# Performance work log

Measured on AMD Instinct MI355X. Metric: run time of the kernel, lower is better.

## Reference

```python
import jax, jax.numpy as jnp
import numpy as np

NDIM, NINEQ, NEQ = 1024, 512, 256
EPS = 1e-4       # Q regularization (module's eps)
N_ITERS = 25     # fixed primal-dual interior-point iterations
SIGMA = 0.1      # centering parameter


def setup_inputs() -> dict:
    key = jax.random.key(0)
    ks = jax.random.split(key, 5)
    L = jnp.tril(jax.random.uniform(ks[0], (NDIM, NDIM)))                      # tril(rand) as in torch init
    q = jax.random.uniform(ks[1], (NDIM,), minval=-1.0, maxval=1.0)
    G = jax.random.uniform(ks[2], (NINEQ, NDIM), minval=-1.0, maxval=1.0)
    A = jax.random.uniform(ks[3], (NEQ, NDIM), minval=-1.0, maxval=1.0)
    b = jax.random.uniform(ks[4], (NEQ,), minval=-1.0, maxval=1.0)
    x0 = jnp.zeros((NDIM,), jnp.float32)   # nn.Parameter(torch.zeros(ndim))
    s0 = jnp.ones((NINEQ,), jnp.float32)   # nn.Parameter(torch.ones(nineq))
    return {"L": L, "q": q, "G": G, "A": A, "b": b, "x0": x0, "s0": s0}


def _frac_to_boundary(v, dv):
    # max step alpha in (0,1] keeping v + alpha*dv > 0, with 0.99 backoff
    safe_dv = jnp.where(dv < 0, dv, -1.0)
    ratio = jnp.where(dv < 0, -v / safe_dv, 1.0)
    return jnp.min(ratio)


def _solve_qp(Q, q, G, h, A, b):
    n, m, p = q.shape[0], h.shape[0], b.shape[0]

    def step(state, _):
        x, s, z, y = state
        r_x = Q @ x + q + G.T @ z + A.T @ y          # dual residual
        r_p = G @ x + s - h                           # primal ineq residual
        r_y = A @ x - b                               # primal eq residual
        mu = jnp.dot(s, z) / m
        r_c = s * z - SIGMA * mu                      # centered complementarity
        D = z / s                                     # diag scaling
        H = Q + G.T @ (D[:, None] * G)                # reduced Hessian [n,n]
        KKT = jnp.block([[H, A.T], [A, jnp.zeros((p, p), Q.dtype)]])
        rhs = jnp.concatenate([-(r_x + G.T @ ((-r_c + z * r_p) / s)), -r_y])
        sol = jnp.linalg.solve(KKT, rhs)
        dx, dy = sol[:n], sol[n:]
        ds = -r_p - G @ dx
        dz = (-r_c - z * ds) / s
        alpha = 0.99 * jnp.minimum(1.0, jnp.minimum(_frac_to_boundary(s, ds), _frac_to_boundary(z, dz)))
        return (x + alpha * dx, s + alpha * ds, z + alpha * dz, y + alpha * dy), None

    init = (jnp.zeros((n,), Q.dtype), jnp.ones((m,), Q.dtype), jnp.ones((m,), Q.dtype), jnp.zeros((p,), Q.dtype))
    (x, s, z, y), _ = jax.lax.scan(step, init, None, length=N_ITERS)
    return x


def reference(L, q, G, A, b, x0, s0):
    Lt = jnp.tril(L)  # M * L with M = tril(ones)
    Q = Lt @ Lt.T + EPS * jnp.eye(L.shape[0], dtype=L.dtype)
    h = G @ x0 + s0   # learn_h branch (source's self.z0 is self.x0)
    return _solve_qp(Q, q, G, h, A, b)
```

## Files before the change

### kernel.cpp

```cpp
#include <hip/hip_runtime.h>
#include <hip/hip_bf16.h>


constexpr int ND = 1024;
constexpr int MI = 512;
constexpr int PE = 256;
constexpr int NM = 512;
constexpr int LDM = 520;
constexpr double EPSQ = 1e-4;
constexpr double SIG = 0.1;
constexpr int NITER = 25;

__device__ __forceinline__ double wred(double v) {
#pragma unroll
  for (int off = 32; off; off >>= 1) v += __shfl_down(v, off, 64);
  return v;
}

__global__ void k_prep(const float* __restrict__ Gf, const float* __restrict__ Af,
                       const float* __restrict__ qf, const float* __restrict__ bf,
                       float* __restrict__ GTf, float* __restrict__ ATf,
                       double* __restrict__ qd, double* __restrict__ bd,
                       double* __restrict__ xv, double* __restrict__ sv,
                       double* __restrict__ zv, double* __restrict__ yv,
// ... 18 lines not shown
  if (wid >= MI) return;
  double acc = 0;
  for (int c = lane; c < ND; c += 64) acc += (double)Gf[(size_t)wid * ND + c] * (double)x0f[c];
  acc = wred(acc);
  if (lane == 0) hd[wid] = acc + (double)s0f[wid];
}

__global__ __launch_bounds__(256) void k_qbuild(const float* __restrict__ Lf,
                                                double* __restrict__ Qd, double* __restrict__ LQ) {
  __shared__ double As[32][33], Bs[32][33];
  int i0 = blockIdx.y * 32, j0 = blockIdx.x * 32;
  int tx = threadIdx.x & 15, ty = threadIdx.x >> 4;
  double acc[2][2] = {};
  int kmax = (i0 < j0 ? i0 : j0) + 32;
  for (int k0 = 0; k0 < kmax; k0 += 32) {
    for (int l = threadIdx.x; l < 1024; l += 256) {
      int r = l >> 5, c = l & 31;
      As[r][c] = (k0 + c <= i0 + r) ? (double)Lf[(size_t)(i0 + r) * ND + k0 + c] : 0.0;
      Bs[r][c] = (k0 + c <= j0 + r) ? (double)Lf[(size_t)(j0 + r) * ND + k0 + c] : 0.0;
    }
    __syncthreads();
#pragma unroll
    for (int k = 0; k < 32; k++) {
      double a0 = As[2 * ty][k], a1 = As[2 * ty + 1][k];
      double b0 = Bs[2 * tx][k], b1 = Bs[2 * tx + 1][k];
      acc[0][0] += a0 * b0; acc[0][1] += a0 * b1;
      acc[1][0] += a1 * b0; acc[1][1] += a1 * b1;
    }
    __syncthreads();
  }
  for (int da = 0; da < 2; da++)
    for (int db = 0; db < 2; db++) {
      int i = i0 + 2 * ty + da, j = j0 + 2 * tx + db;
      double v = acc[da][db] + (i == j ? EPSQ : 0.0);
      Qd[(size_t)i * ND + j] = v;
      LQ[(size_t)i * ND + j] = v;
    }
}

__global__ __launch_bounds__(256) void k_chol_diag_inv(double* __restrict__ A, int lda, int kb,
                                                       double* __restrict__ DG) {
  __shared__ double a[64][65];
  __shared__ double invp[2080];
  __shared__ double dfloor;
  int t = threadIdx.x;
  size_t base = (size_t)kb * 64;
  for (int l = t; l < 4096; l += 256) { int r = l >> 6, c = l & 63; a[r][c] = A[(base + r) * lda + base + c]; }
  __syncthreads();
  if (t == 0) {
    double m = 0;
    for (int i = 0; i < 64; i++) m = fmax(m, fabs(a[i][i]));
    dfloor = m * 1e-28 + 1e-280;
  }
  __syncthreads();
  for (int j = 0; j < 64; j++) {
    if (t == 0) a[j][j] = sqrt(fmax(a[j][j], dfloor));
    __syncthreads();
    double piv = a[j][j];
    for (int r = j + 1 + t; r < 64; r += 256) a[r][j] /= piv;
    __syncthreads();
    int w = 63 - j;
    for (int l = t; l < w * w; l += 256) {
      int rr = j + 1 + l / w, cc = j + 1 + l % w;
      if (cc <= rr) a[rr][cc] -= a[rr][j] * a[cc][j];
    }
    __syncthreads();
  }
  for (int l = t; l < 4096; l += 256) { int r = l >> 6, c = l & 63; if (c <= r) A[(base + r) * lda + base + c] = a[r][c]; }
  if (t < 64) {
    int c = t;
    for (int i = c; i < 64; i++) {
      double v = (i == c) ? 1.0 : 0.0;
      for (int k = c; k < i; k++) v -= a[i][k] * invp[k * (k + 1) / 2 + c];
      invp[i * (i + 1) / 2 + c] = v / a[i][i];
    }
  }
  __syncthreads();
  for (int l = t; l < 4096; l += 256) {
    int r = l >> 6, c = l & 63;
    DG[(size_t)kb * 4096 + (size_t)c * 64 + r] = (c <= r) ? invp[r * (r + 1) / 2 + c] : 0.0;
  }
}

__global__ __launch_bounds__(256) void k_fps(double* __restrict__ A, int lda,
                                             double* __restrict__ PL, int ldp,
                                             double* __restrict__ DG, int kb) {
  extern __shared__ double sh[];
  double* DT = sh;
  double* Bs = sh + 4096;
  double* Pi = sh + 8256;
  double* Pj = sh + 12416;
  const int t = threadIdx.x;
  int idx = blockIdx.x;
  int bi = (int)((sqrtf(8.0f * (float)idx + 1.0f) - 1.0f) * 0.5f);
  while ((bi + 1) * (bi + 2) / 2 <= idx) ++bi;
  while (bi * (bi + 1) / 2 > idx) --bi;
  int bj = idx - bi * (bi + 1) / 2;
  const int ib = kb + 1 + bi, jb = kb + 1 + bj;
  const int tx = t & 15, ty = t >> 4;

  for (int l = t; l < 4096; l += 256) DT[l] = DG[(size_t)kb * 4096 + l];
  for (int l = t; l < 4096; l += 256) { int r = l >> 6, c = l & 63; Bs[r * 65 + c] = A[(size_t)(ib * 64 + r) * lda + kb * 64 + c]; }
  __syncthreads();
  {
    double acc[4][4] = {};
    for (int k = 0; k < 64; ++k) {
      double b0 = Bs[ty * 65 + k], b1 = Bs[(ty + 16) * 65 + k];
      double b2 = Bs[(ty + 32) * 65 + k], b3 = Bs[(ty + 48) * 65 + k];
      double d0 = DT[k * 64 + tx], d1 = DT[k * 64 + tx + 16];
      double d2 = DT[k * 64 + tx + 32], d3 = DT[k * 64 + tx + 48];
      acc[0][0] += b0 * d0; acc[0][1] += b0 * d1; acc[0][2] += b0 * d2; acc[0][3] += b0 * d3;
      acc[1][0] += b1 * d0; acc[1][1] += b1 * d1; acc[1][2] += b1 * d2; acc[1][3] += b1 * d3;
      acc[2][0] += b2 * d0; acc[2][1] += b2 * d1; acc[2][2] += b2 * d2; acc[2][3] += b2 * d3;
      acc[3][0] += b3 * d0; acc[3][1] += b3 * d1; acc[3][2] += b3 * d2; acc[3][3] += b3 * d3;
    }
    __syncthreads();
    for (int e = 0; e < 4; ++e)
      for (int f = 0; f < 4; ++f) Pi[(ty + 16 * e) * 65 + tx + 16 * f] = acc[e][f];
  }
  __syncthreads();
  if (ib == jb) {
    for (int l = t; l < 4096; l += 256) {
      int r = l >> 6, c = l & 63;
      PL[(size_t)(ib * 64 + r) * ldp + kb * 64 + c] = Pi[r * 65 + c];
    }
    double* a = Pj;
    {
      double acc[4][4] = {};
      for (int k = 0; k < 64; ++k) {
        double p0 = Pi[ty * 65 + k], p1 = Pi[(ty + 16) * 65 + k];
        double p2 = Pi[(ty + 32) * 65 + k], p3 = Pi[(ty + 48) * 65 + k];
        double q0 = Pi[tx * 65 + k], q1 = Pi[(tx + 16) * 65 + k];
        double q2 = Pi[(tx + 32) * 65 + k], q3 = Pi[(tx + 48) * 65 + k];
        acc[0][0] += p0 * q0; acc[0][1] += p0 * q1; acc[0][2] += p0 * q2; acc[0][3] += p0 * q3;
        acc[1][0] += p1 * q0; acc[1][1] += p1 * q1; acc[1][2] += p1 * q2; acc[1][3] += p1 * q3;
        acc[2][0] += p2 * q0; acc[2][1] += p2 * q1; acc[2][2] += p2 * q2; acc[2][3] += p2 * q3;
        acc[3][0] += p3 * q0; acc[3][1] += p3 * q1; acc[3][2] += p3 * q2; acc[3][3] += p3 * q3;
      }
      for (int e = 0; e < 4; ++e)
        for (int f = 0; f < 4; ++f) {
          int r = ty + 16 * e, c = tx + 16 * f;
          a[r * 65 + c] = A[(size_t)(ib * 64 + r) * lda + jb * 64 + c] - acc[e][f];
        }
    }
    __syncthreads();
    if (ib == kb + 1) {
      if (t == 0) {
        double m = 0;
        for (int i = 0; i < 64; i++) m = fmax(m, fabs(a[i * 65 + i]));
        sh[16576] = m * 1e-28 + 1e-280;
      }
      __syncthreads();
      double dfloor = sh[16576];
      for (int j = 0; j < 64; ++j) {
        if (t == 0) a[j * 65 + j] = sqrt(fmax(a[j * 65 + j], dfloor));
        __syncthreads();
        double piv = a[j * 65 + j];
        for (int r = j + 1 + t; r < 64; r += 256) a[r * 65 + j] /= piv;
        __syncthreads();
        int w = 63 - j;
        for (int l = t; l < w * w; l += 256) {
          int rr = j + 1 + l / w, cc = j + 1 + l % w;
          if (cc <= rr) a[rr * 65 + cc] -= a[rr * 65 + j] * a[cc * 65 + j];
        }
        __syncthreads();
      }
      double* invp = Bs;
      if (t < 64) {
        int c = t;
        for (int i = c; i < 64; ++i) {
          double v = (i == c) ? 1.0 : 0.0;
          for (int k = c; k < i; ++k) v -= a[i * 65 + k] * invp[k * (k + 1) / 2 + c];
          invp[i * (i + 1) / 2 + c] = v / a[i * 65 + i];
        }
      }
      __syncthreads();
      for (int l = t; l < 4096; l += 256) {
        int r = l >> 6, c = l & 63;
        DG[(size_t)(kb + 1) * 4096 + (size_t)c * 64 + r] = (c <= r) ? invp[r * (r + 1) / 2 + c] : 0.0;
      }
    } else {
      for (int l = t; l < 4096; l += 256) {
        int r = l >> 6, c = l & 63;
        A[(size_t)(ib * 64 + r) * lda + jb * 64 + c] = a[r * 65 + c];
      }
    }
  } else {
    for (int l = t; l < 4096; l += 256) { int r = l >> 6, c = l & 63; Bs[r * 65 + c] = A[(size_t)(jb * 64 + r) * lda + kb * 64 + c]; }
    __syncthreads();
    {
      double acc[4][4] = {};
      for (int k = 0; k < 64; ++k) {
        double b0 = Bs[ty * 65 + k], b1 = Bs[(ty + 16) * 65 + k];
        double b2 = Bs[(ty + 32) * 65 + k], b3 = Bs[(ty + 48) * 65 + k];
        double d0 = DT[k * 64 + tx], d1 = DT[k * 64 + tx + 16];
        double d2 = DT[k * 64 + tx + 32], d3 = DT[k * 64 + tx + 48];
        acc[0][0] += b0 * d0; acc[0][1] += b0 * d1; acc[0][2] += b0 * d2; acc[0][3] += b0 * d3;
        acc[1][0] += b1 * d0; acc[1][1] += b1 * d1; acc[1][2] += b1 * d2; acc[1][3] += b1 * d3;
        acc[2][0] += b2 * d0; acc[2][1] += b2 * d1; acc[2][2] += b2 * d2; acc[2][3] += b2 * d3;
        acc[3][0] += b3 * d0; acc[3][1] += b3 * d1; acc[3][2] += b3 * d2; acc[3][3] += b3 * d3;
      }
      __syncthreads();
      for (int e = 0; e < 4; ++e)
        for (int f = 0; f < 4; ++f) Pj[(ty + 16 * e) * 65 + tx + 16 * f] = acc[e][f];
    }
    __syncthreads();
    double acc[4][4] = {};
    for (int k = 0; k < 64; ++k) {
      double p0 = Pi[ty * 65 + k], p1 = Pi[(ty + 16) * 65 + k];
      double p2 = Pi[(ty + 32) * 65 + k], p3 = Pi[(ty + 48) * 65 + k];
      double q0 = Pj[tx * 65 + k], q1 = Pj[(tx + 16) * 65 + k];
      double q2 = Pj[(tx + 32) * 65 + k], q3 = Pj[(tx + 48) * 65 + k];
      acc[0][0] += p0 * q0; acc[0][1] += p0 * q1; acc[0][2] += p0 * q2; acc[0][3] += p0 * q3;
      acc[1][0] += p1 * q0; acc[1][1] += p1 * q1; acc[1][2] += p1 * q2; acc[1][3] += p1 * q3;
      acc[2][0] += p2 * q0; acc[2][1] += p2 * q1; acc[2][2] += p2 * q2; acc[2][3] += p2 * q3;
      acc[3][0] += p3 * q0; acc[3][1] += p3 * q1; acc[3][2] += p3 * q2; acc[3][3] += p3 * q3;
    }
    for (int e = 0; e < 4; ++e)
      for (int f = 0; f < 4; ++f) {
        int r = ty + 16 * e, c = tx + 16 * f;
        size_t off = (size_t)(ib * 64 + r) * lda + jb * 64 + c;
        A[off] -= acc[e][f];
      }
  }
}

__global__ __launch_bounds__(256) void k_trsmf_g(const double* __restrict__ Lm, int lda,
                                                 double* __restrict__ X, int ldx,
                                                 const double* __restrict__ DG, int kb) {
  __shared__ double Lb[64][64];
  __shared__ double Xs[64][33];
  int t = threadIdx.x;
  int c0 = blockIdx.x * 32;
  int lane2 = t & 31, rbase = t >> 5;
  int row0 = kb * 64;
  double acc[8];
#pragma unroll
  for (int e = 0; e < 8; e++) acc[e] = (row0 + rbase + 8 * e == c0 + lane2) ? 1.0 : 0.0;
  for (int jb = 0; jb < kb; jb++) {
    for (int l = t; l < 4096; l += 256) { int r = l >> 6, c = l & 63; Lb[r][c] = Lm[(size_t)(row0 + r) * lda + jb * 64 + c]; }
    for (int l = t; l < 2048; l += 256) { int k = l >> 5, c = l & 31; Xs[k][c] = X[(size_t)(jb * 64 + k) * ldx + c0 + c]; }
    __syncthreads();
#pragma unroll 4
    for (int k = 0; k < 64; k++) {
      double wv = Xs[k][lane2];
#pragma unroll
      for (int e = 0; e < 8; e++) acc[e] -= Lb[rbase + 8 * e][k] * wv;
    }
    __syncthreads();
  }
  __syncthreads();
#pragma unroll
  for (int e = 0; e < 8; e++) Xs[rbase + 8 * e][lane2] = acc[e];
  for (int l = t; l < 4096; l += 256) Lb[l >> 6][l & 63] = DG[(size_t)kb * 4096 + l];
  __syncthreads();
#pragma unroll
  for (int e = 0; e < 8; e++) {
    int i = rbase + 8 * e;
    double s = 0;
#pragma unroll 4
    for (int k = 0; k < 64; k++) s += Lb[k][i] * Xs[k][lane2];
    X[(size_t)(row0 + i) * ldx + c0 + lane2] = s;
  }
}

__global__ __launch_bounds__(256) void k_trsmb_g(const double* __restrict__ Lm, int lda,
                                                 double* __restrict__ X, int ldx,
                                                 const double* __restrict__ DG, int kb, int nkb) {
  __shared__ double Lb[64][64];
  __shared__ double Xs[64][33];
  int t = threadIdx.x;
  int c0 = blockIdx.x * 32;
  int lane2 = t & 31, rbase = t >> 5;
  int row0 = kb * 64;
  double acc[8];
#pragma unroll
  for (int e = 0; e < 8; e++) acc[e] = X[(size_t)(row0 + rbase + 8 * e) * ldx + c0 + lane2];
  for (int jb = kb + 1; jb < nkb; jb++) {
    for (int l = t; l < 4096; l += 256) { int r = l >> 6, c = l & 63; Lb[r][c] = Lm[(size_t)(jb * 64 + r) * lda + kb * 64 + c]; }
    for (int l = t; l < 2048; l += 256) { int k = l >> 5, c = l & 31; Xs[k][c] = X[(size_t)(jb * 64 + k) * ldx + c0 + c]; }
    __syncthreads();
#pragma unroll 4
    for (int k = 0; k < 64; k++) {
      double wv = Xs[k][lane2];
#pragma unroll
      for (int e = 0; e < 8; e++) acc[e] -= Lb[k][rbase + 8 * e] * wv;
    }
    __syncthreads();
  }
  __syncthreads();
#pragma unroll
  for (int e = 0; e < 8; e++) Xs[rbase + 8 * e][lane2] = acc[e];
  for (int l = t; l < 4096; l += 256) Lb[l >> 6][l & 63] = DG[(size_t)kb * 4096 + l];
  __syncthreads();
#pragma unroll
  for (int e = 0; e < 8; e++) {
    int i = rbase + 8 * e;
    double s = 0;
#pragma unroll 4
    for (int k = 0; k < 64; k++) s += Lb[i][k] * Xs[k][lane2];
    X[(size_t)(row0 + i) * ldx + c0 + lane2] = s;
  }
}

__global__ __launch_bounds__(256) void k_aqi(const float* __restrict__ Af, const double* __restrict__ Qi,
                                             double* __restrict__ AQi) {
// ... 127 lines not shown
    }
    __syncthreads();
  }
  for (int da = 0; da < 2; da++)
    for (int db = 0; db < 2; db++)
      FK0x[(size_t)(g0 + 2 * ty + da) * ND + j0 + 2 * tx + db] = acc[da][db];
}

__global__ __launch_bounds__(256) void k_fk0y(const float* __restrict__ Gf, const double* __restrict__ XY,
                                              double* __restrict__ FK0y) {
  __shared__ double As[32][33], Bs[32][33];
  int b0 = blockIdx.x * 32, g0 = blockIdx.y * 32;
  int tx = threadIdx.x & 15, ty = threadIdx.x >> 4;
  double acc[2][2] = {};
  for (int k0 = 0; k0 < ND; k0 += 32) {
    for (int l = threadIdx.x; l < 1024; l += 256) {
      int r = l >> 5, c = l & 31;
      As[r][c] = (double)Gf[(size_t)(g0 + r) * ND + k0 + c];
      Bs[r][c] = XY[(size_t)(k0 + r) * PE + b0 + c];
    }
    __syncthreads();
#pragma unroll
    for (int k = 0; k < 32; k++) {
      double a0v = As[2 * ty][k], a1v = As[2 * ty + 1][k];
      double b0v = Bs[k][2 * tx], b1v = Bs[k][2 * tx + 1];
      acc[0][0] += a0v * b0v; acc[0][1] += a0v * b1v;
      acc[1][0] += a1v * b0v; acc[1][1] += a1v * b1v;
    }
    __syncthreads();
  }
  for (int da = 0; da < 2; da++)
    for (int db = 0; db < 2; db++)
      FK0y[(size_t)(g0 + 2 * ty + da) * PE + b0 + 2 * tx + db] = acc[da][db];
}

__global__ __launch_bounds__(256) void k_smat(const double* __restrict__ FK0x, const float* __restrict__ Gf,
                                              double* __restrict__ S) {
  __shared__ double As[32][33], Bs[32][33];
  int g0 = blockIdx.y * 32, h0 = blockIdx.x * 32;
  int tx = threadIdx.x & 15, ty = threadIdx.x >> 4;
  double acc[2][2] = {};
  for (int k0 = 0; k0 < ND; k0 += 32) {
    for (int l = threadIdx.x; l < 1024; l += 256) {
      int r = l >> 5, c = l & 31;
      As[r][c] = FK0x[(size_t)(g0 + r) * ND + k0 + c];
      Bs[r][c] = (double)Gf[(size_t)(h0 + r) * ND + k0 + c];
    }
    __syncthreads();
#pragma unroll
    for (int k = 0; k < 32; k++) {
      double a0v = As[2 * ty][k], a1v = As[2 * ty + 1][k];
      double b0v = Bs[2 * tx][k], b1v = Bs[2 * tx + 1][k];
      acc[0][0] += a0v * b0v; acc[0][1] += a0v * b1v;
      acc[1][0] += a1v * b0v; acc[1][1] += a1v * b1v;
    }
    __syncthreads();
  }
  for (int da = 0; da < 2; da++)
    for (int db = 0; db < 2; db++)
      S[(size_t)(g0 + 2 * ty + da) * MI + h0 + 2 * tx + db] = acc[da][db];
}

__global__ __launch_bounds__(256) void k_tr(const double* __restrict__ src, double* __restrict__ dst,
                                            int R, int Cc) {
  __shared__ double tile[32][33];
  int r0 = blockIdx.y * 32, c0 = blockIdx.x * 32;
  for (int l = threadIdx.x; l < 1024; l += 256) {
    int r = l >> 5, c = l & 31;
    tile[r][c] = src[(size_t)(r0 + r) * Cc + c0 + c];
  }
  __syncthreads();
  for (int l = threadIdx.x; l < 1024; l += 256) {
    int r = l >> 5, c = l & 31;
    dst[(size_t)(c0 + r) * R + r0 + c] = tile[c][r];
  }
}

__global__ __launch_bounds__(256) void k_A1(const double* __restrict__ Qd, const float* __restrict__ Gf,
                                            const float* __restrict__ Af, const float* __restrict__ GTf,
                                            const float* __restrict__ ATf, const double* __restrict__ qd,
                                            const double* __restrict__ bd, const double* __restrict__ hd,
                                            const double* __restrict__ xv, const double* __restrict__ sv,
                                            const double* __restrict__ zv, const double* __restrict__ yv,
                                            const double* __restrict__ scal,
                                            double* __restrict__ rxv, double* __restrict__ rp,
                                            double* __restrict__ ry, double* __restrict__ uv,
                                            double* __restrict__ dinv) {
  int lane = threadIdx.x & 63;
  if (blockIdx.x < 256) {
    int wid = blockIdx.x * 4 + (int)(threadIdx.x >> 6);
    double acc = 0;
    for (int k = lane; k < ND; k += 64) acc += Qd[(size_t)wid * ND + k] * xv[k];
    for (int k = lane; k < MI; k += 64) acc += (double)GTf[(size_t)wid * MI + k] * zv[k];
    for (int k = lane; k < PE; k += 64) acc += (double)ATf[(size_t)wid * PE + k] * yv[k];
    acc = wred(acc);
    if (lane == 0) rxv[wid] = acc + qd[wid];
  } else {
    int wid = (blockIdx.x - 256) * 4 + (int)(threadIdx.x >> 6);
    if (wid < MI) {
      double acc = 0;
      for (int c = lane; c < ND; c += 64) acc += (double)Gf[(size_t)wid * ND + c] * xv[c];
      acc = wred(acc);
      if (lane == 0) {
        double s0 = sv[wid], z0 = zv[wid];
        double rpv = acc + s0 - hd[wid];
        rp[wid] = rpv;
        double rc0 = s0 * z0 - SIG * scal[0];
        uv[wid] = (-rc0 + z0 * rpv) / s0;
        dinv[wid] = s0 / z0;
      }
    } else {
      int r = wid - MI;
      double acc = 0;
      for (int c = lane; c < ND; c += 64) acc += (double)Af[(size_t)r * ND + c] * xv[c];
      acc = wred(acc);
      if (lane == 0) ry[r] = acc - bd[r];
    }
  }
}

__global__ __launch_bounds__(256) void k_A2(const double* __restrict__ rxv, const float* __restrict__ GTf,
                                            const double* __restrict__ uv, const double* __restrict__ dinv,
                                            const double* __restrict__ ry, const double* __restrict__ S,
                                            const double* __restrict__ FK0x, const double* __restrict__ FK0y,
                                            double* __restrict__ rhs1, double* __restrict__ Mm) {
  int t = threadIdx.x, lane = t & 63;
  if (blockIdx.x < 256) {
    int wid = blockIdx.x * 4 + (t >> 6);
    double acc = 0;
    for (int k = lane; k < MI; k += 64) acc += (double)GTf[(size_t)wid * MI + k] * uv[k];
    acc = wred(acc);
    if (lane == 0) rhs1[wid] = -(rxv[wid] + acc);
  } else if (blockIdx.x < 320) {
    int rbase = (blockIdx.x - 256) * 8;
    for (int rr = 0; rr < 8; ++rr) {
      int row = rbase + rr;
      for (int c = t; c < NM; c += 256) {
        double v = S[(size_t)row * MI + c];
        if (row == c) v += dinv[row];
        Mm[(size_t)row * LDM + c] = v;
      }
    }
  } else {
    int j = (blockIdx.x - 320) * 4 + (t >> 6);
    double acc = 0;
    for (int k = lane; k < ND; k += 64) acc += FK0x[(size_t)j * ND + k] * rxv[k];
    for (int m = lane; m < MI; m += 64) acc += S[(size_t)j * MI + m] * uv[m];
    for (int c = lane; c < PE; c += 64) acc += FK0y[(size_t)j * PE + c] * ry[c];
    acc = wred(acc);
    if (lane == 0) Mm[(size_t)NM * LDM + j] = -acc;
  }
}

__global__ __launch_bounds__(512) void k_bwdupd(const double* __restrict__ Mm, const double* __restrict__ PL,
                                                const double* __restrict__ DGC, const double* __restrict__ rp,
                                                const double* __restrict__ dinv, double* __restrict__ sv,
                                                double* __restrict__ zv, double* __restrict__ scal,
                                                double* __restrict__ solw) {
  __shared__ double DT[4096];
  __shared__ double g[NM];
  __shared__ double pseg[64];
  __shared__ double acc8[8][64];
  __shared__ double tmp[64];
  __shared__ double red[512];
  __shared__ double dsA[512];
  __shared__ double dzA[512];
  int t = threadIdx.x;
  for (int l = t; l < NM; l += 512) g[l] = Mm[(size_t)NM * LDM + l];
  for (int kbp = 0; kbp < 8; ++kbp) {
    __syncthreads();
    for (int l = t; l < 4096; l += 512) DT[l] = DGC[(size_t)kbp * 4096 + l];
    __syncthreads();
    if (t < 64) {
      double s = 0;
#pragma unroll
      for (int k = 0; k < 64; k++) s += g[kbp * 64 + k] * DT[k * 64 + t];
      pseg[t] = s;
    }
    __syncthreads();
    for (int c = (kbp + 1) * 64 + t; c < NM; c += 512) {
      double s = 0;
#pragma unroll
      for (int k = 0; k < 64; k++) s += pseg[k] * PL[(size_t)c * NM + kbp * 64 + k];
      g[c] -= s;
    }
    if (t < 64) g[kbp * 64 + t] = pseg[t];
  }
  int i8 = t & 63, p8 = t >> 6;
  for (int kb = 7; kb >= 0; --kb) {
    __syncthreads();
    for (int l = t; l < 4096; l += 512) DT[l] = DGC[(size_t)kb * 4096 + l];
    __syncthreads();
    int tr0 = kb * 64 + 64;
    double s = 0;
    for (int rr = p8; rr < NM - tr0; rr += 8)
      s += PL[(size_t)(tr0 + rr) * NM + kb * 64 + i8] * g[tr0 + rr];
    acc8[p8][i8] = s;
    __syncthreads();
    if (t < 64) {
      double v = g[kb * 64 + t];
#pragma unroll
      for (int p = 0; p < 8; p++) v -= acc8[p][t];
      tmp[t] = v;
    }
    __syncthreads();
    if (t < 64) {
      double v = 0;
#pragma unroll
      for (int l = 0; l < 64; l++) v += DT[t * 64 + l] * tmp[l];
      pseg[t] = v;
    }
    __syncthreads();
    if (t < 64) g[kb * 64 + t] = pseg[t];
  }
  __syncthreads();
  solw[t] = g[t];
  double mu = scal[0];
  double s0 = sv[t], z0 = zv[t];
  double ds = -rp[t] - dinv[t] * g[t];
  double rc0 = s0 * z0 - SIG * mu;
  double dz = (-rc0 - z0 * ds) / s0;
  dsA[t] = ds; dzA[t] = dz;
  double rs = (ds < 0.0) ? -s0 / ds : 1.0;
  double rz = (dz < 0.0) ? -z0 / dz : 1.0;
  red[t] = fmin(rs, rz);
  __syncthreads();
  for (int s2 = 256; s2; s2 >>= 1) { if (t < s2) red[t] = fmin(red[t], red[t + s2]); __syncthreads(); }
  double alpha = 0.99 * fmin(1.0, red[0]);
  if (!(alpha == alpha)) alpha = 0.0;
  double us = alpha * dsA[t], uz = alpha * dzA[t];
  if (isfinite(us)) sv[t] += us;
  if (isfinite(uz)) zv[t] += uz;
  __syncthreads();
// ... 18 lines not shown
    for (int m = lane; m < MI; m += 64) acc -= XGT[(size_t)wid * MI + m] * solw[m];
    for (int c = lane; c < PE; c += 64) acc -= XY[(size_t)wid * PE + c] * ry[c];
    acc = wred(acc);
    if (lane == 0) { double u = al * acc; if (isfinite(u)) xv[wid] += u; }
  } else {
    int r = (blockIdx.x - 256) * 4 + (int)(threadIdx.x >> 6);
    double acc = 0;
    for (int k = lane; k < ND; k += 64) acc += YXm[(size_t)r * ND + k] * rhs1[k];
    for (int m = lane; m < MI; m += 64) acc -= YGT[(size_t)r * MI + m] * solw[m];
    for (int c = lane; c < PE; c += 64) acc += SAi[(size_t)r * PE + c] * ry[c];
    acc = wred(acc);
    if (lane == 0) { double u = al * acc; if (isfinite(u)) yv[r] += u; }
  }
}

__global__ void k_out(const double* __restrict__ xv, float* __restrict__ out) {
  int i = blockIdx.x * blockDim.x + threadIdx.x;
  if (i < ND) out[i] = (float)xv[i];
}

__global__ void k_wsdiag(float mb, float* out) {
  int i = blockIdx.x * 256 + threadIdx.x;
  if (i < ND) out[i] = (i == 0 ? (65536.0f * (1.0f + mb)) : 0.0f);
}

extern "C" void kernel_launch(void* const* d_in, const int* in_sizes, int n_in,
                              void* d_out, int out_size, void* d_ws, size_t ws_size,
                              hipStream_t stream) {
  const float* Lf = (const float*)d_in[0];
  const float* qf = (const float*)d_in[1];
  const float* Gf = (const float*)d_in[2];
  const float* Af = (const float*)d_in[3];
  const float* bf = (const float*)d_in[4];
  const float* x0f = (const float*)d_in[5];
  const float* s0f = (const float*)d_in[6];

  double* w = (double*)d_ws;
  double* Qd  = w; w += (size_t)ND * ND;
  double* XX  = w; w += (size_t)ND * ND;
  double* R1  = w; w += (size_t)ND * ND;
  double* R2  = w; w += (size_t)ND * ND;
  double* XY  = w; w += (size_t)ND * PE;
  double* FK0xReg = w; w += (size_t)MI * ND;
  double* SA  = w; w += (size_t)PE * PE;
  double* PLi = w; w += (size_t)NM * NM;
  double* DGH = w; w += (size_t)16 * 4096;
  double* DGA = w; w += (size_t)4 * 4096;
  double* DGC = w; w += (size_t)8 * 4096;
  double* qd = w; w += ND;  double* bd = w; w += PE;  double* hd = w; w += MI;
  double* xv = w; w += ND;  double* sv = w; w += MI;  double* zv = w; w += MI;  double* yv = w; w += PE;
  double* rxv = w; w += ND; double* rp = w; w += MI;  double* ry = w; w += PE;
  double* uv = w; w += MI;  double* dinv = w; w += MI;
  double* rhs1 = w; w += ND; double* solw = w; w += NM;
  double* scal = w; w += 16;
  float* GTf = (float*)w;
  float* ATf = GTf + (size_t)ND * MI;
  char* wend = (char*)(ATf + (size_t)ND * PE);
  size_t need = (size_t)(wend - (char*)d_ws);
  if (ws_size < need) {
    k_wsdiag<<<4, 256, 0, stream>>>((float)(ws_size >> 20), (float*)d_out);
    return;
  }

  double* Qi  = R1;
  double* XGT = R1;
  double* YXm = R1 + (size_t)ND * MI;
  double* YGT = R1 + (size_t)ND * MI + (size_t)PE * ND;
  double* LQ  = R2;
  double* Mm  = R2;
  double* FK0y = R2 + (size_t)(NM + 1) * LDM;
  double* SAi  = FK0y + (size_t)MI * PE;
  double* Smat = SAi + (size_t)PE * PE;
  double* AQi  = FK0xReg;
  double* FK0x = FK0xReg;
  double* PLQ  = XX;
  double* PLA  = XY;

  const size_t ldsFPS = (size_t)16640 * sizeof(double);

  k_prep<<<2048, 256, 0, stream>>>(Gf, Af, qf, bf, GTf, ATf, qd, bd, xv, sv, zv, yv, scal);
  k_h<<<128, 256, 0, stream>>>(Gf, x0f, s0f, hd);
  { dim3 g(32, 32); k_qbuild<<<g, 256, 0, stream>>>(Lf, Qd, LQ); }
  k_chol_diag_inv<<<1, 256, 0, stream>>>(LQ, ND, 0, DGH);
  for (int kb = 0; kb < 15; kb++) {
    int nt = 15 - kb;
    k_fps<<<nt * (nt + 1) / 2, 256, ldsFPS, stream>>>(LQ, ND, PLQ, ND, DGH, kb);
  }
  for (int kb = 0; kb < 16; kb++)  k_trsmf_g<<<32, 256, 0, stream>>>(PLQ, ND, Qi, ND, DGH, kb);
  for (int kb = 15; kb >= 0; kb--) k_trsmb_g<<<32, 256, 0, stream>>>(PLQ, ND, Qi, ND, DGH, kb, 16);
  { dim3 g(32, 8);  k_aqi<<<g, 256, 0, stream>>>(Af, Qi, AQi); }
  { dim3 g(8, 8);   k_sa<<<g, 256, 0, stream>>>(AQi, Af, SA); }
  k_chol_diag_inv<<<1, 256, 0, stream>>>(SA, PE, 0, DGA);
  for (int kb = 0; kb < 3; kb++) {
    int nt = 3 - kb;
    k_fps<<<nt * (nt + 1) / 2, 256, ldsFPS, stream>>>(SA, PE, PLA, PE, DGA, kb);
  }
  for (int kb = 0; kb < 4; kb++)  k_trsmf_g<<<8, 256, 0, stream>>>(PLA, PE, SAi, PE, DGA, kb);
  for (int kb = 3; kb >= 0; kb--) k_trsmb_g<<<8, 256, 0, stream>>>(PLA, PE, SAi, PE, DGA, kb, 4);
  { dim3 g(8, 32);  k_xy<<<g, 256, 0, stream>>>(AQi, SAi, XY); }
  { dim3 g(32, 32); k_xx<<<g, 256, 0, stream>>>(Qi, XY, AQi, XX); }
  { dim3 g(32, 16); k_fk0x<<<g, 256, 0, stream>>>(Gf, XX, FK0x); }
  { dim3 g(8, 16);  k_fk0y<<<g, 256, 0, stream>>>(Gf, XY, FK0y); }
  { dim3 g(16, 16); k_smat<<<g, 256, 0, stream>>>(FK0x, Gf, Smat); }
  { dim3 g(32, 16); k_tr<<<g, 256, 0, stream>>>(FK0x, XGT, MI, ND); }
  { dim3 g(8, 32);  k_tr<<<g, 256, 0, stream>>>(XY, YXm, ND, PE); }
  { dim3 g(8, 16);  k_tr<<<g, 256, 0, stream>>>(FK0y, YGT, MI, PE); }

  for (int it = 0; it < NITER; ++it) {
    k_A1<<<448, 256, 0, stream>>>(Qd, Gf, Af, GTf, ATf, qd, bd, hd, xv, sv, zv, yv, scal,
                                  rxv, rp, ry, uv, dinv);
    k_A2<<<448, 256, 0, stream>>>(rxv, GTf, uv, dinv, ry, Smat, FK0x, FK0y, rhs1, Mm);
    k_chol_diag_inv<<<1, 256, 0, stream>>>(Mm, LDM, 0, DGC);
    for (int kb = 0; kb < 7; kb++) {
      int nt = 7 - kb;
      k_fps<<<nt * (nt + 1) / 2, 256, ldsFPS, stream>>>(Mm, LDM, PLi, NM, DGC, kb);
    }
    k_bwdupd<<<1, 512, 0, stream>>>(Mm, PLi, DGC, rp, dinv, sv, zv, scal, solw);
    k_C<<<320, 256, 0, stream>>>(XX, XGT, XY, YXm, YGT, SAi, rhs1, solw, ry, scal, xv, yv);
  }
  k_out<<<4, 256, 0, stream>>>(xv, (float*)d_out);
}
```

Measured before the change: 39.16 ms.

## Fuse two Cholesky panel steps per launch and fold diag factor into A2

```diff
diff --git a/kernel.cpp b/kernel.cpp
--- a/kernel.cpp
+++ b/kernel.cpp
@@ -124,146 +124,228 @@
   }
 }
 
-__global__ __launch_bounds__(256) void k_fps(double* __restrict__ A, int lda,
-                                             double* __restrict__ PL, int ldp,
-                                             double* __restrict__ DG, int kb) {
+__global__ __launch_bounds__(256) void k_fps2(double* __restrict__ A, int lda,
+                                              double* __restrict__ PL, int ldp,
+                                              double* __restrict__ DG, int kb, int nbk) {
   extern __shared__ double sh[];
-  double* DT = sh;
-  double* Bs = sh + 4096;
-  double* Pi = sh + 8256;
-  double* Pj = sh + 12416;
-  const int t = threadIdx.x;
-  int idx = blockIdx.x;
-  int bi = (int)((sqrtf(8.0f * (float)idx + 1.0f) - 1.0f) * 0.5f);
-  while ((bi + 1) * (bi + 2) / 2 <= idx) ++bi;
-  while (bi * (bi + 1) / 2 > idx) --bi;
-  int bj = idx - bi * (bi + 1) / 2;
-  const int ib = kb + 1 + bi, jb = kb + 1 + bj;
-  const int tx = t & 15, ty = t >> 4;
-
-  for (int l = t; l < 4096; l += 256) DT[l] = DG[(size_t)kb * 4096 + l];
-  for (int l = t; l < 4096; l += 256) { int r = l >> 6, c = l & 63; Bs[r * 65 + c] = A[(size_t)(ib * 64 + r) * lda + kb * 64 + c]; }
-  __syncthreads();
-  {
-    double acc[4][4] = {};
-    for (int k = 0; k < 64; ++k) {
-      double b0 = Bs[ty * 65 + k], b1 = Bs[(ty + 16) * 65 + k];
-      double b2 = Bs[(ty + 32) * 65 + k], b3 = Bs[(ty + 48) * 65 + k];
-      double d0 = DT[k * 64 + tx], d1 = DT[k * 64 + tx + 16];
-      double d2 = DT[k * 64 + tx + 32], d3 = DT[k * 64 + tx + 48];
-      acc[0][0] += b0 * d0; acc[0][1] += b0 * d1; acc[0][2] += b0 * d2; acc[0][3] += b0 * d3;
-      acc[1][0] += b1 * d0; acc[1][1] += b1 * d1; acc[1][2] += b1 * d2; acc[1][3] += b1 * d3;
-      acc[2][0] += b2 * d0; acc[2][1] += b2 * d1; acc[2][2] += b2 * d2; acc[2][3] += b2 * d3;
-      acc[3][0] += b3 * d0; acc[3][1] += b3 * d1; acc[3][2] += b3 * d2; acc[3][3] += b3 * d3;
-    }
-    __syncthreads();
-    for (int e = 0; e < 4; ++e)
-      for (int f = 0; f < 4; ++f) Pi[(ty + 16 * e) * 65 + tx + 16 * f] = acc[e][f];
-  }
-  __syncthreads();
-  if (ib == jb) {
+  double* D  = sh;
+  double* Cb = sh + 4160;
+  double* Pb = sh + 8320;
+  double* Lb = sh + 12480;
+  const int t = threadIdx.x, tx = t & 15, ty = t >> 4;
+  const bool tail = (kb + 2 >= nbk);
+  int bi = 0, bj = 0;
+  if (!tail) {
+    int idx = blockIdx.x;
+    bi = (int)((sqrtf(8.0f * (float)idx + 1.0f) - 1.0f) * 0.5f);
+    while ((bi + 1) * (bi + 2) / 2 <= idx) ++bi;
+    while (bi * (bi + 1) / 2 > idx) --bi;
+    bj = idx - bi * (bi + 1) / 2;
+  }
+  const int ib = kb + 2 + bi, jb = kb + 2 + bj;
+  const bool isDiag = (ib == jb);
+  const bool isBoss = (blockIdx.x == 0);
+
+  double tmp[4][4];
+  auto loadTile = [&](double* dst, int rb, int cb) {
     for (int l = t; l < 4096; l += 256) {
       int r = l >> 6, c = l & 63;
-      PL[(size_t)(ib * 64 + r) * ldp + kb * 64 + c] = Pi[r * 65 + c];
-    }
-    double* a = Pj;
-    {
-      double acc[4][4] = {};
-      for (int k = 0; k < 64; ++k) {
-        double p0 = Pi[ty * 65 + k], p1 = Pi[(ty + 16) * 65 + k];
-        double p2 = Pi[(ty + 32) * 65 + k], p3 = Pi[(ty + 48) * 65 + k];
-        double q0 = Pi[tx * 65 + k], q1 = Pi[(tx + 16) * 65 + k];
-        double q2 = Pi[(tx + 32) * 65 + k], q3 = Pi[(tx + 48) * 65 + k];
-        acc[0][0] += p0 * q0; acc[0][1] += p0 * q1; acc[0][2] += p0 * q2; acc[0][3] += p0 * q3;
-        acc[1][0] += p1 * q0; acc[1][1] += p1 * q1; acc[1][2] += p1 * q2; acc[1][3] += p1 * q3;
-        acc[2][0] += p2 * q0; acc[2][1] += p2 * q1; acc[2][2] += p2 * q2; acc[2][3] += p2 * q3;
-        acc[3][0] += p3 * q0; acc[3][1] += p3 * q1; acc[3][2] += p3 * q2; acc[3][3] += p3 * q3;
-      }
-      for (int e = 0; e < 4; ++e)
-        for (int f = 0; f < 4; ++f) {
-          int r = ty + 16 * e, c = tx + 16 * f;
-          a[r * 65 + c] = A[(size_t)(ib * 64 + r) * lda + jb * 64 + c] - acc[e][f];
-        }
-    }
-    __syncthreads();
-    if (ib == kb + 1) {
-      if (t == 0) {
-        double m = 0;
-        for (int i = 0; i < 64; i++) m = fmax(m, fabs(a[i * 65 + i]));
-        sh[16576] = m * 1e-28 + 1e-280;
+      dst[r * 65 + c] = A[(size_t)(rb * 64 + r) * lda + cb * 64 + c];
+    }
+  };
+  auto mulD = [&](const double* X) {
+#pragma unroll
+    for (int e = 0; e < 4; e++)
+#pragma unroll
+      for (int f = 0; f < 4; f++) tmp[e][f] = 0;
+    for (int k = 0; k < 64; ++k) {
+      double x0 = X[ty * 65 + k], x1 = X[(ty + 16) * 65 + k];
+      double x2 = X[(ty + 32) * 65 + k], x3 = X[(ty + 48) * 65 + k];
+      double d0 = D[k * 64 + tx], d1 = D[k * 64 + tx + 16];
+      double d2 = D[k * 64 + tx + 32], d3 = D[k * 64 + tx + 48];
+      tmp[0][0] += x0 * d0; tmp[0][1] += x0 * d1; tmp[0][2] += x0 * d2; tmp[0][3] += x0 * d3;
+      tmp[1][0] += x1 * d0; tmp[1][1] += x1 * d1; tmp[1][2] += x1 * d2; tmp[1][3] += x1 * d3;
+      tmp[2][0] += x2 * d0; tmp[2][1] += x2 * d1; tmp[2][2] += x2 * d2; tmp[2][3] += x2 * d3;
+      tmp[3][0] += x3 * d0; tmp[3][1] += x3 * d1; tmp[3][2] += x3 * d2; tmp[3][3] += x3 * d3;
+    }
+  };
+  auto mulNT = [&](const double* X, const double* Y) {
+#pragma unroll
+    for (int e = 0; e < 4; e++)
+#pragma unroll
+      for (int f = 0; f < 4; f++) tmp[e][f] = 0;
+    for (int k = 0; k < 64; ++k) {
+      double x0 = X[ty * 65 + k], x1 = X[(ty + 16) * 65 + k];
+      double x2 = X[(ty + 32) * 65 + k], x3 = X[(ty + 48) * 65 + k];
+      double y0 = Y[tx * 65 + k], y1 = Y[(tx + 16) * 65 + k];
+      double y2 = Y[(tx + 32) * 65 + k], y3 = Y[(tx + 48) * 65 + k];
+      tmp[0][0] += x0 * y0; tmp[0][1] += x0 * y1; tmp[0][2] += x0 * y2; tmp[0][3] += x0 * y3;
+      tmp[1][0] += x1 * y0; tmp[1][1] += x1 * y1; tmp[1][2] += x1 * y2; tmp[1][3] += x1 * y3;
+      tmp[2][0] += x2 * y0; tmp[2][1] += x2 * y1; tmp[2][2] += x2 * y2; tmp[2][3] += x2 * y3;
+      tmp[3][0] += x3 * y0; tmp[3][1] += x3 * y1; tmp[3][2] += x3 * y2; tmp[3][3] += x3 * y3;
+    }
+  };
+  auto storeTmp = [&](double* dst) {
+    __syncthreads();
+#pragma unroll
+    for (int e = 0; e < 4; e++)
+#pragma unroll
+      for (int f = 0; f < 4; f++) dst[(ty + 16 * e) * 65 + tx + 16 * f] = tmp[e][f];
+    __syncthreads();
+  };
+  auto factorD = [&](int dgout) {
+    if (t == 0) {
+      double m = 0;
+      for (int i2 = 0; i2 < 64; i2++) m = fmax(m, fabs(D[i2 * 65 + i2]));
+      D[4159] = m * 1e-28 + 1e-280;
+    }
+    __syncthreads();
+    double dfl = D[4159];
+    for (int j = 0; j < 64; ++j) {
+      if (t == 0) D[j * 65 + j] = sqrt(fmax(D[j * 65 + j], dfl));
+      __syncthreads();
+      double piv = D[j * 65 + j];
+      for (int r = j + 1 + t; r < 64; r += 256) D[r * 65 + j] /= piv;
+      __syncthreads();
+      int w = 63 - j;
+      for (int l = t; l < w * w; l += 256) {
+        int rr = j + 1 + l / w, cc = j + 1 + l % w;
+        if (cc <= rr) D[rr * 65 + cc] -= D[rr * 65 + j] * D[cc * 65 + j];
       }
       __syncthreads();
-      double dfloor = sh[16576];
-      for (int j = 0; j < 64; ++j) {
-        if (t == 0) a[j * 65 + j] = sqrt(fmax(a[j * 65 + j], dfloor));
-        __syncthreads();
-        double piv = a[j * 65 + j];
-        for (int r = j + 1 + t; r < 64; r += 256) a[r * 65 + j] /= piv;
-        __syncthreads();
-        int w = 63 - j;
-        for (int l = t; l < w * w; l += 256) {
-          int rr = j + 1 + l / w, cc = j + 1 + l % w;
-          if (cc <= rr) a[rr * 65 + cc] -= a[rr * 65 + j] * a[cc * 65 + j];
-        }
-        __syncthreads();
+    }
+    double* invp = Cb;
+    if (t < 64) {
+      int c = t;
+      for (int i2 = c; i2 < 64; ++i2) {
+        double v = (i2 == c) ? 1.0 : 0.0;
+        for (int k = c; k < i2; ++k) v -= D[i2 * 65 + k] * invp[k * (k + 1) / 2 + c];
+        invp[i2 * (i2 + 1) / 2 + c] = v / D[i2 * 65 + i2];
       }
-      double* invp = Bs;
-      if (t < 64) {
-        int c = t;
-        for (int i = c; i < 64; ++i) {
-          double v = (i == c) ? 1.0 : 0.0;
-          for (int k = c; k < i; ++k) v -= a[i * 65 + k] * invp[k * (k + 1) / 2 + c];
-          invp[i * (i + 1) / 2 + c] = v / a[i * 65 + i];
-        }
-      }
-      __syncthreads();
-      for (int l = t; l < 4096; l += 256) {
-        int r = l >> 6, c = l & 63;
-        DG[(size_t)(kb + 1) * 4096 + (size_t)c * 64 + r] = (c <= r) ? invp[r * (r + 1) / 2 + c] : 0.0;
-      }
-    } else {
-      for (int l = t; l < 4096; l += 256) {
-        int r = l >> 6, c = l & 63;
-        A[(size_t)(ib * 64 + r) * lda + jb * 64 + c] = a[r * 65 + c];
-      }
-    }
+    }
+    __syncthreads();
+    for (int l = t; l < 4096; l += 256) {
+      int k = l >> 6, c = l & 63;
+      D[k * 64 + c] = (k <= c) ? invp[c * (c + 1) / 2 + k] : 0.0;
+    }
+    __syncthreads();
+    if (dgout >= 0 && isBoss)
+      for (int l = t; l < 4096; l += 256) DG[(size_t)dgout * 4096 + l] = D[l];
+    __syncthreads();
+  };
+
+  for (int l = t; l < 4096; l += 256) D[l] = DG[(size_t)kb * 4096 + l];
+  __syncthreads();
+
+  if (tail) {
+    loadTile(Lb, kb + 1, kb);
+    __syncthreads();
+    mulD(Lb); storeTmp(Cb);
+    for (int l = t; l < 4096; l += 256) {
+      int r = l >> 6, c = l & 63;
+      PL[(size_t)((kb + 1) * 64 + r) * ldp + kb * 64 + c] = Cb[r * 65 + c];
+    }
+    mulNT(Cb, Cb);
+    __syncthreads();
+#pragma unroll
+    for (int e = 0; e < 4; e++)
+#pragma unroll
+      for (int f = 0; f < 4; f++)
+        D[(ty + 16 * e) * 65 + tx + 16 * f] =
+            A[(size_t)((kb + 1) * 64 + ty + 16 * e) * lda + (kb + 1) * 64 + tx + 16 * f] - tmp[e][f];
+    __syncthreads();
+    factorD(kb + 1);
+    return;
+  }
+
+  double acc[4][4];
+#pragma unroll
+  for (int e = 0; e < 4; e++)
+#pragma unroll
+    for (int f = 0; f < 4; f++)
+      acc[e][f] = A[(size_t)(ib * 64 + ty + 16 * e) * lda + jb * 64 + tx + 16 * f];
+
+  loadTile(Lb, kb + 1, kb);
+  __syncthreads();
+  mulD(Lb); storeTmp(Cb);
+  if (isBoss)
+    for (int l = t; l < 4096; l += 256) {
+      int r = l >> 6, c = l & 63;
+      PL[(size_t)((kb + 1) * 64 + r) * ldp + kb * 64 + c] = Cb[r * 65 + c];
+    }
+  loadTile(Lb, ib, kb);
+  __syncthreads();
+  mulD(Lb); storeTmp(Pb);
+  if (isDiag)
+    for (int l = t; l < 4096; l += 256) {
+      int r = l >> 6, c = l & 63;
+      PL[(size_t)(ib * 64 + r) * ldp + kb * 64 + c] = Pb[r * 65 + c];
+    }
+  if (!isDiag) {
+    loadTile(Lb, jb, kb);
+    __syncthreads();
+    mulD(Lb); storeTmp(Lb);
+  }
+  const double* Pj0 = isDiag ? Pb : Lb;
+  mulNT(Pb, Pj0);
+#pragma unroll
+  for (int e = 0; e < 4; e++)
+#pragma unroll
+    for (int f = 0; f < 4; f++) acc[e][f] -= tmp[e][f];
+  mulNT(Pb, Cb);
+#pragma unroll
+  for (int e = 0; e < 4; e++)
+#pragma unroll
+    for (int f = 0; f < 4; f++)
+      tmp[e][f] = A[(size_t)(ib * 64 + ty + 16 * e) * lda + (kb + 1) * 64 + tx + 16 * f] - tmp[e][f];
+  storeTmp(Pb);
+  if (!isDiag) {
+    mulNT(Lb, Cb);
+#pragma unroll
+    for (int e = 0; e < 4; e++)
+#pragma unroll
+      for (int f = 0; f < 4; f++)
+        tmp[e][f] = A[(size_t)(jb * 64 + ty + 16 * e) * lda + (kb + 1) * 64 + tx + 16 * f] - tmp[e][f];
+    storeTmp(Lb);
+  }
+  mulNT(Cb, Cb);
+  __syncthreads();
+#pragma unroll
+  for (int e = 0; e < 4; e++)
+#pragma unroll
+    for (int f = 0; f < 4; f++)
+      D[(ty + 16 * e) * 65 + tx + 16 * f] =
+          A[(size_t)((kb + 1) * 64 + ty + 16 * e) * lda + (kb + 1) * 64 + tx + 16 * f] - tmp[e][f];
+  __syncthreads();
+  factorD(kb + 1);
+  mulD(Pb); storeTmp(Pb);
+  if (isDiag)
+    for (int l = t; l < 4096; l += 256) {
+      int r = l >> 6, c = l & 63;
+      PL[(size_t)(ib * 64 + r) * ldp + (kb + 1) * 64 + c] = Pb[r * 65 + c];
+    }
+  if (!isDiag) { mulD(Lb); storeTmp(Lb); }
+  const double* Pj1 = isDiag ? Pb : Lb;
+  mulNT(Pb, Pj1);
+#pragma unroll
+  for (int e = 0; e < 4; e++)
+#pragma unroll
+    for (int f = 0; f < 4; f++) acc[e][f] -= tmp[e][f];
+
+  if (isBoss) {
+    __syncthreads();
+#pragma unroll
+    for (int e = 0; e < 4; e++)
+#pragma unroll
+      for (int f = 0; f < 4; f++) D[(ty + 16 * e) * 65 + tx + 16 * f] = acc[e][f];
+    __syncthreads();
+    factorD(kb + 2);
   } else {
-    for (int l = t; l < 4096; l += 256) { int r = l >> 6, c = l & 63; Bs[r * 65 + c] = A[(size_t)(jb * 64 + r) * lda + kb * 64 + c]; }
-    __syncthreads();
-    {
-      double acc[4][4] = {};
-      for (int k = 0; k < 64; ++k) {
-        double b0 = Bs[ty * 65 + k], b1 = Bs[(ty + 16) * 65 + k];
-        double b2 = Bs[(ty + 32) * 65 + k], b3 = Bs[(ty + 48) * 65 + k];
-        double d0 = DT[k * 64 + tx], d1 = DT[k * 64 + tx + 16];
-        double d2 = DT[k * 64 + tx + 32], d3 = DT[k * 64 + tx + 48];
-        acc[0][0] += b0 * d0; acc[0][1] += b0 * d1; acc[0][2] += b0 * d2; acc[0][3] += b0 * d3;
-        acc[1][0] += b1 * d0; acc[1][1] += b1 * d1; acc[1][2] += b1 * d2; acc[1][3] += b1 * d3;
-        acc[2][0] += b2 * d0; acc[2][1] += b2 * d1; acc[2][2] += b2 * d2; acc[2][3] += b2 * d3;
-        acc[3][0] += b3 * d0; acc[3][1] += b3 * d1; acc[3][2] += b3 * d2; acc[3][3] += b3 * d3;
-      }
-      __syncthreads();
-      for (int e = 0; e < 4; ++e)
-        for (int f = 0; f < 4; ++f) Pj[(ty + 16 * e) * 65 + tx + 16 * f] = acc[e][f];
-    }
-    __syncthreads();
-    double acc[4][4] = {};
-    for (int k = 0; k < 64; ++k) {
-      double p0 = Pi[ty * 65 + k], p1 = Pi[(ty + 16) * 65 + k];
-      double p2 = Pi[(ty + 32) * 65 + k], p3 = Pi[(ty + 48) * 65 + k];
-      double q0 = Pj[tx * 65 + k], q1 = Pj[(tx + 16) * 65 + k];
-      double q2 = Pj[(tx + 32) * 65 + k], q3 = Pj[(tx + 48) * 65 + k];
-      acc[0][0] += p0 * q0; acc[0][1] += p0 * q1; acc[0][2] += p0 * q2; acc[0][3] += p0 * q3;
-      acc[1][0] += p1 * q0; acc[1][1] += p1 * q1; acc[1][2] += p1 * q2; acc[1][3] += p1 * q3;
-      acc[2][0] += p2 * q0; acc[2][1] += p2 * q1; acc[2][2] += p2 * q2; acc[2][3] += p2 * q3;
-      acc[3][0] += p3 * q0; acc[3][1] += p3 * q1; acc[3][2] += p3 * q2; acc[3][3] += p3 * q3;
-    }
-    for (int e = 0; e < 4; ++e)
-      for (int f = 0; f < 4; ++f) {
-        int r = ty + 16 * e, c = tx + 16 * f;
-        size_t off = (size_t)(ib * 64 + r) * lda + jb * 64 + c;
-        A[off] -= acc[e][f];
-      }
+#pragma unroll
+    for (int e = 0; e < 4; e++)
+#pragma unroll
+      for (int f = 0; f < 4; f++)
+        A[(size_t)(ib * 64 + ty + 16 * e) * lda + jb * 64 + tx + 16 * f] = acc[e][f];
   }
 }
 
@@ -557,21 +639,21 @@
                                             const double* __restrict__ bd, const double* __restrict__ hd,
                                             const double* __restrict__ xv, const double* __restrict__ sv,
                                             const double* __restrict__ zv, const double* __restrict__ yv,
-                                            const double* __restrict__ scal,
+                                            const double* __restrict__ scal, const double* __restrict__ S,
                                             double* __restrict__ rxv, double* __restrict__ rp,
                                             double* __restrict__ ry, double* __restrict__ uv,
-                                            double* __restrict__ dinv) {
-  int lane = threadIdx.x & 63;
+                                            double* __restrict__ dinv, double* __restrict__ Mm) {
+  int t = threadIdx.x, lane = t & 63;
   if (blockIdx.x < 256) {
-    int wid = blockIdx.x * 4 + (int)(threadIdx.x >> 6);
+    int wid = blockIdx.x * 4 + (t >> 6);
     double acc = 0;
     for (int k = lane; k < ND; k += 64) acc += Qd[(size_t)wid * ND + k] * xv[k];
     for (int k = lane; k < MI; k += 64) acc += (double)GTf[(size_t)wid * MI + k] * zv[k];
     for (int k = lane; k < PE; k += 64) acc += (double)ATf[(size_t)wid * PE + k] * yv[k];
     acc = wred(acc);
     if (lane == 0) rxv[wid] = acc + qd[wid];
-  } else {
-    int wid = (blockIdx.x - 256) * 4 + (int)(threadIdx.x >> 6);
+  } else if (blockIdx.x < 448) {
+    int wid = (blockIdx.x - 256) * 4 + (t >> 6);
     if (wid < MI) {
       double acc = 0;
       for (int c = lane; c < ND; c += 64) acc += (double)Gf[(size_t)wid * ND + c] * xv[c];
@@ -591,14 +673,25 @@
       acc = wred(acc);
       if (lane == 0) ry[r] = acc - bd[r];
     }
+  } else {
+    int rbase = (blockIdx.x - 448) * 8;
+    for (int rr = 0; rr < 8; ++rr) {
+      int row = rbase + rr;
+      for (int c = t; c < NM; c += 256) {
+        double v = S[(size_t)row * MI + c];
+        if (row == c) v += sv[row] / zv[row];
+        Mm[(size_t)row * LDM + c] = v;
+      }
+    }
   }
 }
 
 __global__ __launch_bounds__(256) void k_A2(const double* __restrict__ rxv, const float* __restrict__ GTf,
-                                            const double* __restrict__ uv, const double* __restrict__ dinv,
-                                            const double* __restrict__ ry, const double* __restrict__ S,
-                                            const double* __restrict__ FK0x, const double* __restrict__ FK0y,
-                                            double* __restrict__ rhs1, double* __restrict__ Mm) {
+                                            const double* __restrict__ uv, const double* __restrict__ ry,
+                                            const double* __restrict__ S, const double* __restrict__ FK0x,
+                                            const double* __restrict__ FK0y, double* __restrict__ rhs1,
+                                            double* __restrict__ Mm, double* __restrict__ DGC) {
+  __shared__ double sh2[6241];
   int t = threadIdx.x, lane = t & 63;
   if (blockIdx.x < 256) {
     int wid = blockIdx.x * 4 + (t >> 6);
@@ -606,24 +699,52 @@
     for (int k = lane; k < MI; k += 64) acc += (double)GTf[(size_t)wid * MI + k] * uv[k];
     acc = wred(acc);
     if (lane == 0) rhs1[wid] = -(rxv[wid] + acc);
-  } else if (blockIdx.x < 320) {
-    int rbase = (blockIdx.x - 256) * 8;
-    for (int rr = 0; rr < 8; ++rr) {
-      int row = rbase + rr;
-      for (int c = t; c < NM; c += 256) {
-        double v = S[(size_t)row * MI + c];
-        if (row == c) v += dinv[row];
-        Mm[(size_t)row * LDM + c] = v;
-      }
-    }
-  } else {
-    int j = (blockIdx.x - 320) * 4 + (t >> 6);
+  } else if (blockIdx.x < 384) {
+    int j = (blockIdx.x - 256) * 4 + (t >> 6);
     double acc = 0;
     for (int k = lane; k < ND; k += 64) acc += FK0x[(size_t)j * ND + k] * rxv[k];
     for (int m = lane; m < MI; m += 64) acc += S[(size_t)j * MI + m] * uv[m];
     for (int c = lane; c < PE; c += 64) acc += FK0y[(size_t)j * PE + c] * ry[c];
     acc = wred(acc);
     if (lane == 0) Mm[(size_t)NM * LDM + j] = -acc;
+  } else {
+    double* a = sh2;
+    double* invp = sh2 + 4160;
+    for (int l = t; l < 4096; l += 256) { int r = l >> 6, c = l & 63; a[r * 65 + c] = Mm[(size_t)r * LDM + c]; }
+    __syncthreads();
+    if (t == 0) {
+      double m = 0;
+      for (int i = 0; i < 64; i++) m = fmax(m, fabs(a[i * 65 + i]));
+      sh2[6240] = m * 1e-28 + 1e-280;
+    }
+    __syncthreads();
+    double dfl = sh2[6240];
+    for (int j = 0; j < 64; j++) {
+      if (t == 0) a[j * 65 + j] = sqrt(fmax(a[j * 65 + j], dfl));
+      __syncthreads();
+      double piv = a[j * 65 + j];
+      for (int r = j + 1 + t; r < 64; r += 256) a[r * 65 + j] /= piv;
+      __syncthreads();
+      int w = 63 - j;
+      for (int l = t; l < w * w; l += 256) {
+        int rr = j + 1 + l / w, cc = j + 1 + l % w;
+        if (cc <= rr) a[rr * 65 + cc] -= a[rr * 65 + j] * a[cc * 65 + j];
+      }
+      __syncthreads();
+    }
+    if (t < 64) {
+      int c = t;
+      for (int i = c; i < 64; i++) {
+        double v = (i == c) ? 1.0 : 0.0;
+        for (int k = c; k < i; k++) v -= a[i * 65 + k] * invp[k * (k + 1) / 2 + c];
+        invp[i * (i + 1) / 2 + c] = v / a[i * 65 + i];
+      }
+    }
+    __syncthreads();
+    for (int l = t; l < 4096; l += 256) {
+      int r = l >> 6, c = l & 63;
+      DGC[(size_t)c * 64 + r] = (c <= r) ? invp[r * (r + 1) / 2 + c] : 0.0;
+    }
   }
 }
 
@@ -808,18 +929,20 @@
   k_h<<<128, 256, 0, stream>>>(Gf, x0f, s0f, hd);
   { dim3 g(32, 32); k_qbuild<<<g, 256, 0, stream>>>(Lf, Qd, LQ); }
   k_chol_diag_inv<<<1, 256, 0, stream>>>(LQ, ND, 0, DGH);
-  for (int kb = 0; kb < 15; kb++) {
-    int nt = 15 - kb;
-    k_fps<<<nt * (nt + 1) / 2, 256, ldsFPS, stream>>>(LQ, ND, PLQ, ND, DGH, kb);
+  for (int kb = 0; kb < 16; kb += 2) {
+    int T = 16 - kb - 2;
+    int grid = (T > 0) ? T * (T + 1) / 2 : 1;
+    k_fps2<<<grid, 256, ldsFPS, stream>>>(LQ, ND, PLQ, ND, DGH, kb, 16);
   }
   for (int kb = 0; kb < 16; kb++)  k_trsmf_g<<<32, 256, 0, stream>>>(PLQ, ND, Qi, ND, DGH, kb);
   for (int kb = 15; kb >= 0; kb--) k_trsmb_g<<<32, 256, 0, stream>>>(PLQ, ND, Qi, ND, DGH, kb, 16);
   { dim3 g(32, 8);  k_aqi<<<g, 256, 0, stream>>>(Af, Qi, AQi); }
   { dim3 g(8, 8);   k_sa<<<g, 256, 0, stream>>>(AQi, Af, SA); }
   k_chol_diag_inv<<<1, 256, 0, stream>>>(SA, PE, 0, DGA);
-  for (int kb = 0; kb < 3; kb++) {
-    int nt = 3 - kb;
-    k_fps<<<nt * (nt + 1) / 2, 256, ldsFPS, stream>>>(SA, PE, PLA, PE, DGA, kb);
+  for (int kb = 0; kb < 4; kb += 2) {
+    int T = 4 - kb - 2;
+    int grid = (T > 0) ? T * (T + 1) / 2 : 1;
+    k_fps2<<<grid, 256, ldsFPS, stream>>>(SA, PE, PLA, PE, DGA, kb, 4);
   }
   for (int kb = 0; kb < 4; kb++)  k_trsmf_g<<<8, 256, 0, stream>>>(PLA, PE, SAi, PE, DGA, kb);
   for (int kb = 3; kb >= 0; kb--) k_trsmb_g<<<8, 256, 0, stream>>>(PLA, PE, SAi, PE, DGA, kb, 4);
@@ -833,13 +956,13 @@
   { dim3 g(8, 16);  k_tr<<<g, 256, 0, stream>>>(FK0y, YGT, MI, PE); }
 
   for (int it = 0; it < NITER; ++it) {
-    k_A1<<<448, 256, 0, stream>>>(Qd, Gf, Af, GTf, ATf, qd, bd, hd, xv, sv, zv, yv, scal,
-                                  rxv, rp, ry, uv, dinv);
-    k_A2<<<448, 256, 0, stream>>>(rxv, GTf, uv, dinv, ry, Smat, FK0x, FK0y, rhs1, Mm);
-    k_chol_diag_inv<<<1, 256, 0, stream>>>(Mm, LDM, 0, DGC);
-    for (int kb = 0; kb < 7; kb++) {
-      int nt = 7 - kb;
-      k_fps<<<nt * (nt + 1) / 2, 256, ldsFPS, stream>>>(Mm, LDM, PLi, NM, DGC, kb);
+    k_A1<<<512, 256, 0, stream>>>(Qd, Gf, Af, GTf, ATf, qd, bd, hd, xv, sv, zv, yv, scal,
+                                  Smat, rxv, rp, ry, uv, dinv, Mm);
+    k_A2<<<385, 256, 0, stream>>>(rxv, GTf, uv, ry, Smat, FK0x, FK0y, rhs1, Mm, DGC);
+    for (int kb = 0; kb < 8; kb += 2) {
+      int T = 8 - kb - 2;
+      int grid = (T > 0) ? T * (T + 1) / 2 : 1;
+      k_fps2<<<grid, 256, ldsFPS, stream>>>(Mm, LDM, PLi, NM, DGC, kb, 8);
     }
     k_bwdupd<<<1, 512, 0, stream>>>(Mm, PLi, DGC, rp, dinv, sv, zv, scal, solw);
     k_C<<<320, 256, 0, stream>>>(XX, XGT, XY, YXm, YGT, SAi, rhs1, solw, ry, scal, xv, yv);
```

After: 40.68 ms. +3.9%, slower.
